# Kernel optimization log

Measured on AMD Instinct MI355X. Metric: run time of the kernel, lower is better.

The kernel has to match this reference:

```python
import jax, jax.numpy as jnp
import numpy as np

FEAT_DIM = 2048
NUM_CLASSES = 1000
BATCH = 8192
REACH_SCALE = 10.0
COS_SCALE = 16.0


def setup_inputs() -> dict:
    key = jax.random.key(0)
    ks = jax.random.split(key, 7)
    x = jax.random.normal(ks[0], (BATCH, FEAT_DIM), dtype=jnp.float32)
    centroids = jax.random.normal(ks[1], (NUM_CLASSES, FEAT_DIM), dtype=jnp.float32)
    # nn.Linear-style params (W: [out, in], b: [out]), small init scale
    s_h = 1.0 / np.sqrt(FEAT_DIM)
    W_hall = jax.random.uniform(ks[2], (NUM_CLASSES, FEAT_DIM), jnp.float32, -s_h, s_h)
    b_hall = jax.random.uniform(ks[3], (NUM_CLASSES,), jnp.float32, -s_h, s_h)
    W_sel = jax.random.uniform(ks[4], (FEAT_DIM, FEAT_DIM), jnp.float32, -s_h, s_h)
    b_sel = jax.random.uniform(ks[5], (FEAT_DIM,), jnp.float32, -s_h, s_h)
    # CosNorm_Classifier weight: [num_classes, feat_dim]
    W_cos = jax.random.uniform(ks[6], (NUM_CLASSES, FEAT_DIM), jnp.float32, -s_h, s_h)
    return {"x": x, "centroids": centroids, "W_hall": W_hall, "b_hall": b_hall,
            "W_sel": W_sel, "b_sel": b_sel, "W_cos": W_cos}


def reference(x, centroids, W_hall, b_hall, W_sel, b_sel, W_cos):
    # --- min Euclidean distance to centroids via the matmul identity ---
    x_sq = jnp.sum(x * x, axis=1, keepdims=True)               # [B, 1]
    c_sq = jnp.sum(centroids * centroids, axis=1)[None, :]     # [1, C]
    d2 = x_sq + c_sq - 2.0 * (x @ centroids.T)                 # [B, C]
    min_dist = jnp.sqrt(jnp.maximum(jnp.min(d2, axis=1), 0.0)) # [B]
    reachability = (REACH_SCALE / min_dist)[:, None]           # [B, 1] (broadcasts over feat)

    # --- hallucinated memory attention over class centroids ---
    values_memory = jax.nn.softmax(x @ W_hall.T + b_hall, axis=1)  # [B, C]
    memory_feature = values_memory @ centroids                     # [B, D]

    # --- gated fusion ---
    concept_selector = jnp.tanh(x @ W_sel.T + b_sel)               # [B, D]
    infused_feature = concept_selector * memory_feature            # [B, D]
    fused = reachability * (x + infused_feature)                   # [B, D]

    # --- CosNorm classifier: scale * (|x|/(1+|x|)) * (x/|x|) @ (W/|W|)^T ---
    norm_x = jnp.linalg.norm(fused, axis=1, keepdims=True)         # [B, 1]
    ex = (norm_x / (1.0 + norm_x)) * (fused / norm_x)              # [B, D]
    ew = W_cos / jnp.linalg.norm(W_cos, axis=1, keepdims=True)     # [C, D]
    logits = COS_SCALE * (ex @ ew.T)                               # [B, C]

    direct_feature = x
    return logits, direct_feature, infused_feature
```

## Files before the change

### kernel.cpp

```cpp
#include <hip/hip_runtime.h>
#include <hip/hip_bf16.h>

typedef __bf16 bf16x8 __attribute__((ext_vector_type(8)));
typedef float  f32x4  __attribute__((ext_vector_type(4)));
typedef unsigned short u16;

__device__ __forceinline__ u16 f2bf(float f) {
    __hip_bfloat16 h = __float2bfloat16(f);
    return __builtin_bit_cast(unsigned short, h);
}
__device__ __forceinline__ float bf2f(u16 u) {
    return __bfloat162float(__builtin_bit_cast(__hip_bfloat16, u));
}
__device__ __forceinline__ float fast_tanh(float x) {
    float e = __expf(2.f * x);
    return 1.f - 2.f / (e + 1.f);
}

template <int MODE>
__device__ __forceinline__ float blockReduce(float v, float* sbuf) {
    #pragma unroll
    for (int off = 32; off > 0; off >>= 1) {
        float o = __shfl_down(v, off, 64);
        v = (MODE == 0) ? v + o : (MODE == 1) ? fmaxf(v, o) : fminf(v, o);
    }
    int lane = threadIdx.x & 63, w = threadIdx.x >> 6;
    __syncthreads();
    if (lane == 0) sbuf[w] = v;
    __syncthreads();
    float r = sbuf[0];
    #pragma unroll
    for (int i = 1; i < 4; ++i) {
        float o = sbuf[i];
        r = (MODE == 0) ? r + o : (MODE == 1) ? fmaxf(r, o) : fminf(r, o);
    }
    return r;
}

__global__ void convert_x(const float* __restrict__ src, u16* __restrict__ dst,
                          float* __restrict__ rowsq, float* __restrict__ copyOut,
                          float* __restrict__ scaleAcc) {
    __shared__ float sbuf[4];
    int r = blockIdx.x, t = threadIdx.x;
    size_t base = (size_t)r * 2048 + t * 8;
    float4 a0 = *(const float4*)(src + base);
    float4 a1 = *(const float4*)(src + base + 4);
    float ss = a0.x*a0.x + a0.y*a0.y + a0.z*a0.z + a0.w*a0.w
             + a1.x*a1.x + a1.y*a1.y + a1.z*a1.z + a1.w*a1.w;
    ushort4 u0, u1;
    u0.x = f2bf(a0.x); u0.y = f2bf(a0.y); u0.z = f2bf(a0.z); u0.w = f2bf(a0.w);
    u1.x = f2bf(a1.x); u1.y = f2bf(a1.y); u1.z = f2bf(a1.z); u1.w = f2bf(a1.w);
    *(ushort4*)(dst + base)     = u0;
    *(ushort4*)(dst + base + 4) = u1;
    *(float4*)(copyOut + base)     = a0;
    *(float4*)(copyOut + base + 4) = a1;
    ss = blockReduce<0>(ss, sbuf);
    if (t == 0) {
        rowsq[r] = ss;
        scaleAcc[r] = 0.f;
    }
}

__global__ void convert_weights(const float* __restrict__ cent, const float* __restrict__ whall,
                                const float* __restrict__ wsel, u16* __restrict__ Bp,
                                float* __restrict__ csq,
                                const float* __restrict__ wcos, u16* __restrict__ ew) {
    __shared__ float sbuf[4];
    int r = blockIdx.x, t = threadIdx.x;
    if (r >= 4096) {
        int rr = r - 4096;
        size_t base = (size_t)rr * 2048 + t * 8;
        ushort4 u0 = {0,0,0,0}, u1 = {0,0,0,0};
        if (rr < 1000) {
            float4 a0 = *(const float4*)(wcos + base);
            float4 a1 = *(const float4*)(wcos + base + 4);
            float ss = a0.x*a0.x + a0.y*a0.y + a0.z*a0.z + a0.w*a0.w
                     + a1.x*a1.x + a1.y*a1.y + a1.z*a1.z + a1.w*a1.w;
            ss = blockReduce<0>(ss, sbuf);
            float sc = 1.f / sqrtf(ss);
            u0.x = f2bf(a0.x*sc); u0.y = f2bf(a0.y*sc); u0.z = f2bf(a0.z*sc); u0.w = f2bf(a0.w*sc);
            u1.x = f2bf(a1.x*sc); u1.y = f2bf(a1.y*sc); u1.z = f2bf(a1.z*sc); u1.w = f2bf(a1.w*sc);
        }
        *(ushort4*)(ew + base)     = u0;
        *(ushort4*)(ew + base + 4) = u1;
        return;
    }
    const float* src; int sr; bool valid;
    if (r < 1024)       { src = cent;  sr = r;        valid = sr < 1000; }
    else if (r < 2048)  { src = whall; sr = r - 1024; valid = sr < 1000; }
    else                { src = wsel;  sr = r - 2048; valid = true; }
    size_t dbase = (size_t)r * 2048 + t * 8;
    float ss = 0.f;
    ushort4 u0 = {0,0,0,0}, u1 = {0,0,0,0};
    if (valid) {
        size_t sbase = (size_t)sr * 2048 + t * 8;
        float4 a0 = *(const float4*)(src + sbase);
        float4 a1 = *(const float4*)(src + sbase + 4);
        ss = a0.x*a0.x + a0.y*a0.y + a0.z*a0.z + a0.w*a0.w
           + a1.x*a1.x + a1.y*a1.y + a1.z*a1.z + a1.w*a1.w;
        u0.x = f2bf(a0.x); u0.y = f2bf(a0.y); u0.z = f2bf(a0.z); u0.w = f2bf(a0.w);
        u1.x = f2bf(a1.x); u1.y = f2bf(a1.y); u1.z = f2bf(a1.z); u1.w = f2bf(a1.w);
    }
    *(ushort4*)(Bp + dbase)     = u0;
    *(ushort4*)(Bp + dbase + 4) = u1;
    if (r < 1024) {
        ss = blockReduce<0>(ss, sbuf);
        if (t == 0) csq[r] = ss;
    }
}

__global__ void transpose_to_bf16(const float* __restrict__ src, u16* __restrict__ dst, int validRows) {
    __shared__ u16 tile[32][33];
    int d0 = blockIdx.x * 32;
    int c0 = blockIdx.y * 32;
    int tx = threadIdx.x, ty = threadIdx.y;
    #pragma unroll
    for (int k = 0; k < 4; ++k) {
        int c = c0 + ty + k * 8;
        float v = (c < validRows) ? src[(size_t)c * 2048 + d0 + tx] : 0.f;
        tile[ty + k * 8][tx] = f2bf(v);
    }
    __syncthreads();
    #pragma unroll
    for (int k = 0; k < 4; ++k) {
        int d = d0 + ty + k * 8;
        dst[(size_t)d * 1024 + c0 + tx] = tile[tx][ty + k * 8];
    }
}

template <int EPI>
__global__ __launch_bounds__(256, 4)
void gemm_bt(const u16* __restrict__ A, const u16* __restrict__ Bt,
             float* __restrict__ Cf, u16* __restrict__ Cb,
             int K, int lda, int ldc, int nValid,
             const float* __restrict__ bias,
             const u16* __restrict__ selp, int ldsel,
             const float* __restrict__ reach, const u16* __restrict__ xh2,
             u16* __restrict__ fusedh, float* __restrict__ scaleAcc) {
    __shared__ u16 As[128 * 64];
    __shared__ u16 Bs[128 * 64];
    const int tid  = threadIdx.x;
    const int lane = tid & 63;
    const int w    = tid >> 6;
    const int wr   = w >> 1, wc = w & 1;
    const int quad = lane >> 4, r16 = lane & 15;
    const int sw   = r16 & 7;
    const int lr   = lane >> 3;
    const int lc   = lane & 7;
    const int lk   = (lc ^ lr) * 8;
    const size_t rowBase = (size_t)blockIdx.y * 128;
    const size_t colBase = (size_t)blockIdx.x * 128;
    const int kOff = blockIdx.z * K;

    f32x4 acc[4][4] = {};

    for (int kt = 0; kt < K; kt += 64) {
        #pragma unroll
        for (int i = 0; i < 4; ++i) {
            int ci = w * 4 + i;
            const u16* ga = A  + (rowBase + ci * 8 + lr) * (size_t)lda + kOff + kt + lk;
            const u16* gb = Bt + (colBase + ci * 8 + lr) * (size_t)lda + kOff + kt + lk;
            __builtin_amdgcn_global_load_lds(
                (const __attribute__((address_space(1))) void*)ga,
                (__attribute__((address_space(3))) void*)(As + ci * 512), 16, 0, 0);
            __builtin_amdgcn_global_load_lds(
                (const __attribute__((address_space(1))) void*)gb,
                (__attribute__((address_space(3))) void*)(Bs + ci * 512), 16, 0, 0);
        }
        __syncthreads();
        #pragma unroll
        for (int kk2 = 0; kk2 < 2; ++kk2) {
            const int off = (((kk2 << 2) | quad) ^ sw) * 8;
            bf16x8 a[4], b[4];
            #pragma unroll
            for (int i = 0; i < 4; ++i)
                a[i] = *(const bf16x8*)(As + (wr * 64 + i * 16 + r16) * 64 + off);
            #pragma unroll
            for (int j = 0; j < 4; ++j)
                b[j] = *(const bf16x8*)(Bs + (wc * 64 + j * 16 + r16) * 64 + off);
            #pragma unroll
            for (int i = 0; i < 4; ++i)
                #pragma unroll
                for (int j = 0; j < 4; ++j)
                    acc[i][j] = __builtin_amdgcn_mfma_f32_16x16x32_bf16(a[i], b[j], acc[i][j], 0, 0, 0);
        }
        __syncthreads();
    }

    if (EPI == 2) {
        #pragma unroll
        for (int i = 0; i < 4; ++i) {
            #pragma unroll
            for (int v = 0; v < 4; ++v) {
                size_t grow = rowBase + wr * 64 + i * 16 + quad * 4 + v;
                float rch = reach[grow];
                float rs = 0.f;
                #pragma unroll
                for (int j = 0; j < 4; ++j) {
                    size_t gcol = colBase + wc * 64 + j * 16 + r16;
                    float val = acc[i][j][v];
                    float sv  = bf2f(selp[grow * (size_t)ldsel + gcol]);
                    float t   = fast_tanh(sv + bias[gcol]);
                    float inf = t * val;
                    Cf[grow * (size_t)ldc + gcol] = inf;
                    float xv = bf2f(xh2[grow * (size_t)ldc + gcol]);
                    float fs = rch * (xv + inf);
                    fusedh[grow * (size_t)ldc + gcol] = f2bf(fs);
                    rs += fs * fs;
                }
                #pragma unroll
                for (int off = 8; off > 0; off >>= 1)
                    rs += __shfl_down(rs, off, 16);
                if (r16 == 0) atomicAdd(&scaleAcc[grow], rs);
            }
        }
    } else {
        #pragma unroll
        for (int i = 0; i < 4; ++i) {
            #pragma unroll
            for (int j = 0; j < 4; ++j) {
                #pragma unroll
                for (int v = 0; v < 4; ++v) {
                    size_t grow = rowBase + wr * 64 + i * 16 + quad * 4 + v;
                    size_t gcol = colBase + wc * 64 + j * 16 + r16;
                    float val = acc[i][j][v];
                    if (EPI == 1) {
                        Cb[grow * (size_t)ldc + gcol] = f2bf(val);
                    } else if (EPI == 3) {
                        if ((int)gcol < nValid) {
                            float sc = 16.f / (1.f + sqrtf(bias[grow]));
                            atomicAdd(&Cf[grow * (size_t)ldc + gcol], sc * val);
                        }
                    }
                }
            }
        }
    }
}

__global__ void min_softmax(const u16* __restrict__ Sp, const float* __restrict__ xsq,
                            const float* __restrict__ csq, const float* __restrict__ bh,
                            float* __restrict__ reach, u16* __restrict__ Vm,
                            float* __restrict__ outLog) {
    __shared__ float sbuf[4];
    int r = blockIdx.x, t = threadIdx.x;
    size_t rb = (size_t)r * 4096;
    int c0 = t * 4;
    if (t < 250) {
        float4 z = {0.f, 0.f, 0.f, 0.f};
        *(float4*)(outLog + (size_t)r * 1000 + c0) = z;
    }
    float m = 1e30f;
    if (t < 250) {
        ushort4 d4 = *(const ushort4*)(Sp + rb + c0);
        float4 cq = *(const float4*)(csq + c0);
        m = fminf(fminf(cq.x - 2.f * bf2f(d4.x), cq.y - 2.f * bf2f(d4.y)),
                  fminf(cq.z - 2.f * bf2f(d4.z), cq.w - 2.f * bf2f(d4.w)));
    }
    m = blockReduce<2>(m, sbuf);
    if (t == 0) {
        float d2 = xsq[r] + m;
        reach[r] = 10.f / sqrtf(fmaxf(d2, 0.f));
    }
    float l[4];
    float mx = -1e30f;
    if (t < 250) {
        ushort4 h4 = *(const ushort4*)(Sp + rb + 1024 + c0);
        float4 b4 = *(const float4*)(bh + c0);
        l[0] = bf2f(h4.x) + b4.x;
        l[1] = bf2f(h4.y) + b4.y;
        l[2] = bf2f(h4.z) + b4.z;
        l[3] = bf2f(h4.w) + b4.w;
        mx = fmaxf(fmaxf(l[0], l[1]), fmaxf(l[2], l[3]));
    } else {
        l[0] = l[1] = l[2] = l[3] = -1e30f;
    }
    mx = blockReduce<1>(mx, sbuf);
    float s = 0.f;
    #pragma unroll
    for (int i = 0; i < 4; ++i) {
        l[i] = (t < 250) ? __expf(l[i] - mx) : 0.f;
        s += l[i];
    }
    s = blockReduce<0>(s, sbuf);
    float inv = 1.f / s;
    ushort4 o;
    o.x = f2bf(l[0] * inv); o.y = f2bf(l[1] * inv);
    o.z = f2bf(l[2] * inv); o.w = f2bf(l[3] * inv);
    *(ushort4*)(Vm + (size_t)r * 1024 + c0) = o;
}

extern "C" void kernel_launch(void* const* d_in, const int* in_sizes, int n_in,
                              void* d_out, int out_size, void* d_ws, size_t ws_size,
                              hipStream_t stream) {
    const float* x      = (const float*)d_in[0];
    const float* cent   = (const float*)d_in[1];
    const float* W_hall = (const float*)d_in[2];
    const float* b_hall = (const float*)d_in[3];
    const float* W_sel  = (const float*)d_in[4];
    const float* b_sel  = (const float*)d_in[5];
    const float* W_cos  = (const float*)d_in[6];

    float* out_logits = (float*)d_out;
    float* out_x      = out_logits + (size_t)8192 * 1000;
    float* out_inf    = out_x      + (size_t)8192 * 2048;

    char* ws = (char*)d_ws;
    u16*   xh     = (u16*)  (ws);
    u16*   Bp     = (u16*)  (ws + 33554432);
    u16*   ew     = (u16*)  (ws + 50331648);
    u16*   centT  = (u16*)  (ws + 54525952);
    u16*   Sp     = (u16*)  (ws + 58720256);
    u16*   Vm     = (u16*)  (ws + 125829120);
    u16*   fusedh = (u16*)  (ws + 142606336);
    float* xsq    = (float*)(ws + 176160768);
    float* csq    = (float*)(ws + 176193536);
    float* reach  = (float*)(ws + 176197632);
    float* scale  = (float*)(ws + 176230400);

    (void)in_sizes; (void)n_in; (void)out_size; (void)ws_size;

    convert_x<<<8192, 256, 0, stream>>>(x, xh, xsq, out_x, scale);
    convert_weights<<<5120, 256, 0, stream>>>(cent, W_hall, W_sel, Bp, csq, W_cos, ew);
    transpose_to_bf16<<<dim3(64, 32), dim3(32, 8), 0, stream>>>(cent, centT, 1000);

    gemm_bt<1><<<dim3(32, 64), 256, 0, stream>>>(xh, Bp, nullptr, Sp, 2048, 2048, 4096, 0,
                                                 nullptr, nullptr, 0, nullptr, nullptr, nullptr, nullptr);
    min_softmax<<<8192, 256, 0, stream>>>(Sp, xsq, csq, b_hall, reach, Vm, out_logits);

    gemm_bt<2><<<dim3(16, 64), 256, 0, stream>>>(Vm, centT, out_inf, nullptr, 1024, 1024, 2048, 0,
                                                 b_sel, Sp + 2048, 4096, reach, xh, fusedh, scale);

    gemm_bt<3><<<dim3(8, 64, 2), 256, 0, stream>>>(fusedh, ew, out_logits, nullptr, 1024, 2048, 1000, 1000,
                                                   scale, nullptr, 0, nullptr, nullptr, nullptr, nullptr);
}
```

Before: 567.9 us.

## Replace split-K atomic logits GEMM with 64-row tile kernel and direct stores

The final cosine-classifier GEMM used to split K into two halves and accumulate into the logits with float atomics, which meant min_softmax had to zero the logits first. A new kernel with 64x128 tiles now runs the full K=2048 per block and writes scaled results with plain stores, and the zeroing pass is removed from min_softmax. The grid keeps the same block count, just split over rows instead of K. In exchange, each block runs a longer K loop with a smaller A tile, so data reuse per block is lower.

```diff
diff --git a/kernel.cpp b/kernel.cpp
--- a/kernel.cpp
+++ b/kernel.cpp
@@ -132,7 +132,7 @@
 __global__ __launch_bounds__(256, 4)
 void gemm_bt(const u16* __restrict__ A, const u16* __restrict__ Bt,
              float* __restrict__ Cf, u16* __restrict__ Cb,
-             int K, int lda, int ldc, int nValid,
+             int K, int ldc,
              const float* __restrict__ bias,
              const u16* __restrict__ selp, int ldsel,
              const float* __restrict__ reach, const u16* __restrict__ xh2,
@@ -150,7 +150,6 @@
     const int lk   = (lc ^ lr) * 8;
     const size_t rowBase = (size_t)blockIdx.y * 128;
     const size_t colBase = (size_t)blockIdx.x * 128;
-    const int kOff = blockIdx.z * K;
 
     f32x4 acc[4][4] = {};
 
@@ -158,8 +157,8 @@
         #pragma unroll
         for (int i = 0; i < 4; ++i) {
             int ci = w * 4 + i;
-            const u16* ga = A  + (rowBase + ci * 8 + lr) * (size_t)lda + kOff + kt + lk;
-            const u16* gb = Bt + (colBase + ci * 8 + lr) * (size_t)lda + kOff + kt + lk;
+            const u16* ga = A  + (rowBase + ci * 8 + lr) * (size_t)K + kt + lk;
+            const u16* gb = Bt + (colBase + ci * 8 + lr) * (size_t)K + kt + lk;
             __builtin_amdgcn_global_load_lds(
                 (const __attribute__((address_space(1))) void*)ga,
                 (__attribute__((address_space(3))) void*)(As + ci * 512), 16, 0, 0);
@@ -223,33 +222,92 @@
                 for (int v = 0; v < 4; ++v) {
                     size_t grow = rowBase + wr * 64 + i * 16 + quad * 4 + v;
                     size_t gcol = colBase + wc * 64 + j * 16 + r16;
-                    float val = acc[i][j][v];
-                    if (EPI == 1) {
-                        Cb[grow * (size_t)ldc + gcol] = f2bf(val);
-                    } else if (EPI == 3) {
-                        if ((int)gcol < nValid) {
-                            float sc = 16.f / (1.f + sqrtf(bias[grow]));
-                            atomicAdd(&Cf[grow * (size_t)ldc + gcol], sc * val);
-                        }
-                    }
+                    Cb[grow * (size_t)ldc + gcol] = f2bf(acc[i][j][v]);
                 }
             }
         }
     }
 }
 
+__global__ __launch_bounds__(256, 4)
+void gemm_c64(const u16* __restrict__ A, const u16* __restrict__ Bt,
+              float* __restrict__ Cf, int K, int ldc, int nValid,
+              const float* __restrict__ bias) {
+    __shared__ u16 As[64 * 64];
+    __shared__ u16 Bs[128 * 64];
+    const int tid  = threadIdx.x;
+    const int lane = tid & 63;
+    const int w    = tid >> 6;
+    const int quad = lane >> 4, r16 = lane & 15;
+    const int sw   = r16 & 7;
+    const int lr   = lane >> 3;
+    const int lc   = lane & 7;
+    const int lk   = (lc ^ lr) * 8;
+    const size_t rowBase = (size_t)blockIdx.y * 64;
+    const size_t colBase = (size_t)blockIdx.x * 128;
+
+    f32x4 acc[4][2] = {};
+
+    for (int kt = 0; kt < K; kt += 64) {
+        #pragma unroll
+        for (int i = 0; i < 2; ++i) {
+            int ci = w * 2 + i;
+            const u16* ga = A + (rowBase + ci * 8 + lr) * (size_t)K + kt + lk;
+            __builtin_amdgcn_global_load_lds(
+                (const __attribute__((address_space(1))) void*)ga,
+                (__attribute__((address_space(3))) void*)(As + ci * 512), 16, 0, 0);
+        }
+        #pragma unroll
+        for (int i = 0; i < 4; ++i) {
+            int ci = w * 4 + i;
+            const u16* gb = Bt + (colBase + ci * 8 + lr) * (size_t)K + kt + lk;
+            __builtin_amdgcn_global_load_lds(
+                (const __attribute__((address_space(1))) void*)gb,
+                (__attribute__((address_space(3))) void*)(Bs + ci * 512), 16, 0, 0);
+        }
+        __syncthreads();
+        #pragma unroll
+        for (int kk2 = 0; kk2 < 2; ++kk2) {
+            const int off = (((kk2 << 2) | quad) ^ sw) * 8;
+            bf16x8 a[4], b[2];
+            #pragma unroll
+            for (int i = 0; i < 4; ++i)
+                a[i] = *(const bf16x8*)(As + (i * 16 + r16) * 64 + off);
+            #pragma unroll
+            for (int j = 0; j < 2; ++j)
+                b[j] = *(const bf16x8*)(Bs + (w * 32 + j * 16 + r16) * 64 + off);
+            #pragma unroll
+            for (int i = 0; i < 4; ++i)
+                #pragma unroll
+                for (int j = 0; j < 2; ++j)
+                    acc[i][j] = __builtin_amdgcn_mfma_f32_16x16x32_bf16(a[i], b[j], acc[i][j], 0, 0, 0);
+        }
+        __syncthreads();
+    }
+
+    #pragma unroll
+    for (int i = 0; i < 4; ++i) {
+        #pragma unroll
+        for (int v = 0; v < 4; ++v) {
+            size_t grow = rowBase + i * 16 + quad * 4 + v;
+            float sc = 16.f / (1.f + sqrtf(bias[grow]));
+            #pragma unroll
+            for (int j = 0; j < 2; ++j) {
+                size_t gcol = colBase + w * 32 + j * 16 + r16;
+                if ((int)gcol < nValid)
+                    Cf[grow * (size_t)ldc + gcol] = sc * acc[i][j][v];
+            }
+        }
+    }
+}
+
 __global__ void min_softmax(const u16* __restrict__ Sp, const float* __restrict__ xsq,
                             const float* __restrict__ csq, const float* __restrict__ bh,
-                            float* __restrict__ reach, u16* __restrict__ Vm,
-                            float* __restrict__ outLog) {
+                            float* __restrict__ reach, u16* __restrict__ Vm) {
     __shared__ float sbuf[4];
     int r = blockIdx.x, t = threadIdx.x;
     size_t rb = (size_t)r * 4096;
     int c0 = t * 4;
-    if (t < 250) {
-        float4 z = {0.f, 0.f, 0.f, 0.f};
-        *(float4*)(outLog + (size_t)r * 1000 + c0) = z;
-    }
     float m = 1e30f;
     if (t < 250) {
         ushort4 d4 = *(const ushort4*)(Sp + rb + c0);
@@ -324,13 +382,12 @@
     convert_weights<<<5120, 256, 0, stream>>>(cent, W_hall, W_sel, Bp, csq, W_cos, ew);
     transpose_to_bf16<<<dim3(64, 32), dim3(32, 8), 0, stream>>>(cent, centT, 1000);
 
-    gemm_bt<1><<<dim3(32, 64), 256, 0, stream>>>(xh, Bp, nullptr, Sp, 2048, 2048, 4096, 0,
+    gemm_bt<1><<<dim3(32, 64), 256, 0, stream>>>(xh, Bp, nullptr, Sp, 2048, 4096,
                                                  nullptr, nullptr, 0, nullptr, nullptr, nullptr, nullptr);
-    min_softmax<<<8192, 256, 0, stream>>>(Sp, xsq, csq, b_hall, reach, Vm, out_logits);
-
-    gemm_bt<2><<<dim3(16, 64), 256, 0, stream>>>(Vm, centT, out_inf, nullptr, 1024, 1024, 2048, 0,
+    min_softmax<<<8192, 256, 0, stream>>>(Sp, xsq, csq, b_hall, reach, Vm);
+
+    gemm_bt<2><<<dim3(16, 64), 256, 0, stream>>>(Vm, centT, out_inf, nullptr, 1024, 2048,
                                                  b_sel, Sp + 2048, 4096, reach, xh, fusedh, scale);
 
-    gemm_bt<3><<<dim3(8, 64, 2), 256, 0, stream>>>(fusedh, ew, out_logits, nullptr, 1024, 2048, 1000, 1000,
-                                                   scale, nullptr, 0, nullptr, nullptr, nullptr, nullptr);
-}
+    gemm_c64<<<dim3(8, 128), 256, 0, stream>>>(fusedh, ew, out_logits, 2048, 1000, 1000, scale);
+}
```

Measured after the change: 504.7 us. 1.13x faster.
